# Optimization experiments

Measured on AMD Instinct MI355X. Metric: run time of the kernel, lower is better.

The kernel has to match this reference:

```python
import jax, jax.numpy as jnp
import numpy as np

B, S, E, H = 4, 2048, 1024, 16
D = E // H  # head_dim = 64
ROPE_BASE = 10000.0


def _rope(x):
    # x: [B, H, S, D] -> rotary position embedding applied over seq dim
    seq_len = x.shape[2]
    inv_freq = 1.0 / (ROPE_BASE ** (jnp.arange(0, D, 2, dtype=jnp.float32) / D))  # [D/2]
    freqs = jnp.arange(seq_len, dtype=jnp.float32)[:, None] * inv_freq[None, :]   # [S, D/2]
    emb = jnp.concatenate([freqs, freqs], axis=-1)                                 # [S, D]
    cos = jnp.cos(emb).astype(x.dtype)
    sin = jnp.sin(emb).astype(x.dtype)
    x1, x2 = jnp.split(x, 2, axis=-1)
    rotated = jnp.concatenate([-x2, x1], axis=-1)
    return x * cos + rotated * sin


def setup_inputs() -> dict:
    key = jax.random.key(0)
    ks = jax.random.split(key, 10)
    p = 0.02
    return {
        "x": jax.random.normal(ks[0], (B, S, E), dtype=jnp.float32),
        "Wq": jax.random.normal(ks[1], (E, E), dtype=jnp.float32) * p,
        "bq": jnp.zeros((E,), dtype=jnp.float32),
        "Wk": jax.random.normal(ks[2], (E, E), dtype=jnp.float32) * p,
        "bk": jnp.zeros((E,), dtype=jnp.float32),
        "Wv": jax.random.normal(ks[3], (E, E), dtype=jnp.float32) * p,
        "bv": jnp.zeros((E,), dtype=jnp.float32),
        "Wo": jax.random.normal(ks[4], (E, E), dtype=jnp.float32) * p,
        "bo": jnp.zeros((E,), dtype=jnp.float32),
        "key_padding_mask": jnp.zeros((B, S), dtype=bool),
    }


def reference(x, Wq, bq, Wk, bk, Wv, bv, Wo, bo, key_padding_mask):
    b, s, _ = x.shape
    # QKV projections -> [B, H, S, D]
    def proj(W, bias):
        return (x @ W + bias).reshape(b, s, H, D).transpose(0, 2, 1, 3)
    q = _rope(proj(Wq, bq))
    k = _rope(proj(Wk, bk))
    v = proj(Wv, bv)
    scale = D ** -0.5
    scores = jnp.einsum('bhqd,bhkd->bhqk', q, k) * scale  # [B, H, S, S]
    scores = jnp.where(key_padding_mask[:, None, None, :], jnp.finfo(scores.dtype).min, scores)
    probs = jax.nn.softmax(scores, axis=-1)
    out = jnp.einsum('bhqk,bhkd->bhqd', probs, v)         # [B, H, S, D]
    out = out.transpose(0, 2, 1, 3).reshape(b, s, E)
    return out @ Wo + bo
```

## Files before the change

### kernel.cpp

```cpp
#include <hip/hip_runtime.h>
#include <hip/hip_bf16.h>
#include <math.h>

#define Bn 4
#define Sn 2048
#define En 1024
#define Hn 16
#define Dn 64
#define Mn (Bn * Sn)

typedef __attribute__((ext_vector_type(8))) short short8;
typedef __attribute__((ext_vector_type(4))) short short4v;
typedef __attribute__((ext_vector_type(4))) float f32x4;
typedef __attribute__((ext_vector_type(16))) float f32x16;

#if __has_builtin(__builtin_amdgcn_exp2f)
#define EXP2(x) __builtin_amdgcn_exp2f(x)
#else
#define EXP2(x) exp2f(x)
#endif

#define GLOAD16(g, s) __builtin_amdgcn_global_load_lds( \
    (const __attribute__((address_space(1))) unsigned int*)(g), \
    (__attribute__((address_space(3))) unsigned int*)(s), 16, 0, 0)

__device__ inline unsigned short f2bf(float f) {
    unsigned int u = __float_as_uint(f);
    u += 0x7FFFu + ((u >> 16) & 1u);
    return (unsigned short)(u >> 16);
}
__device__ inline float bf2f(unsigned short h) {
    return __uint_as_float(((unsigned int)h) << 16);
}
__device__ inline void split2(float f, unsigned short& hi, unsigned short& lo) {
    hi = f2bf(f);
    lo = f2bf(f - bf2f(hi));
}
__device__ inline short8 ld8s(const unsigned short* p) {
    union { short4v h[2]; short8 v; } r;
    r.h[0] = *(const short4v*)p;
    r.h[1] = *(const short4v*)(p + 4);
    return r.v;
}
__device__ inline short8 g8(const unsigned short* p) {
    union { int4 i; short8 v; } r;
    r.i = *(const int4*)p;
    return r.v;
}

__device__ inline void st16(unsigned short* base, int row, int col16, int4 v) {
    const unsigned off = ((unsigned)(row * 128 + col16 * 2)) ^ ((unsigned)((row & 7) << 4));
    *(int4*)((char*)base + off) = v;
}
__device__ inline short8 ld16(const unsigned short* base, int row, int col16) {
    const unsigned off = ((unsigned)(row * 128 + col16 * 2)) ^ ((unsigned)((row & 7) << 4));
    union { int4 i; short8 v; } r;
    r.i = *(const int4*)((const char*)base + off);
    return r.v;
}

__global__ void rope_table_kernel(float* __restrict__ ct, float* __restrict__ st) {
    int i = blockIdx.x * blockDim.x + threadIdx.x;
    if (i < Sn * 32) {
        int s = i >> 5, p = i & 31;
        double inv = pow(10000.0, -(double)p / 32.0);
        double a = (double)s * inv;
        ct[i] = (float)cos(a);
        st[i] = (float)sin(a);
    }
}

__global__ __launch_bounds__(256) void convx_kernel(
    const float* __restrict__ X, unsigned short* __restrict__ Xh) {
    int i = blockIdx.x * 256 + threadIdx.x;
    float4 v = ((const float4*)X)[i];
    float f[4] = {v.x, v.y, v.z, v.w};
    short4v h;
#pragma unroll
    for (int j = 0; j < 4; ++j) h[j] = (short)f2bf(f[j]);
    ((short4v*)Xh)[i] = h;
}

__global__ __launch_bounds__(256) void tconv_kernel(
    const float* __restrict__ W, unsigned short* __restrict__ WhT,
    int rowLen, int dup) {
    __shared__ float Ws[64][65];
    const int t = threadIdx.x;
    const int kb = blockIdx.y * 64, nb = blockIdx.x * 64;
    const int lr = t >> 2, lc = (t & 3) * 16;
#pragma unroll
    for (int u = 0; u < 4; ++u) {
        float4 v = *(const float4*)&W[(size_t)(kb + lr) * En + nb + lc + 4 * u];
        Ws[lr][lc + 4 * u + 0] = v.x; Ws[lr][lc + 4 * u + 1] = v.y;
        Ws[lr][lc + 4 * u + 2] = v.z; Ws[lr][lc + 4 * u + 3] = v.w;
    }
    __syncthreads();
    const int orow = t >> 2, ock = (t & 3) * 16;
#pragma unroll
    for (int u = 0; u < 4; ++u) {
        short4v hs;
#pragma unroll
        for (int j = 0; j < 4; ++j) hs[j] = (short)f2bf(Ws[ock + 4 * u + j][orow]);
        unsigned short* dst = &WhT[(size_t)(nb + orow) * rowLen + kb + ock + 4 * u];
        *(short4v*)dst = hs;
        if (dup) *(short4v*)(dst + 1024) = hs;
    }
}

__global__ __launch_bounds__(256) void vtrans_kernel(
    const unsigned short* __restrict__ Vb, unsigned short* __restrict__ VbT) {
    __shared__ unsigned short Ts[64][68];
    const int t = threadIdx.x;
    const int bh = blockIdx.y;
    const int s0 = blockIdx.x * 64;
    const size_t ibase = (size_t)bh * Sn * Dn;
    const int lr = t >> 2, lc = (t & 3) * 16;
    int4 i0 = *(const int4*)&Vb[ibase + (size_t)(s0 + lr) * Dn + lc];
    int4 i1 = *(const int4*)&Vb[ibase + (size_t)(s0 + lr) * Dn + lc + 8];
    *(int2*)&Ts[lr][lc] = make_int2(i0.x, i0.y);
    *(int2*)&Ts[lr][lc + 4] = make_int2(i0.z, i0.w);
    *(int2*)&Ts[lr][lc + 8] = make_int2(i1.x, i1.y);
    *(int2*)&Ts[lr][lc + 12] = make_int2(i1.z, i1.w);
    __syncthreads();
    const int dr = t >> 2, sc = (t & 3) * 16;
    unsigned short o[16];
#pragma unroll
    for (int j = 0; j < 16; ++j) o[j] = Ts[sc + j][dr];
    unsigned short* op = &VbT[(size_t)bh * Dn * Sn + (size_t)dr * Sn + s0 + sc];
    *(int4*)&op[0] = *(int4*)&o[0];
    *(int4*)&op[8] = *(int4*)&o[8];
}

template <int KN, int EPI>
__global__ __launch_bounds__(256) void gemm97(
    const unsigned short* __restrict__ A, const unsigned short* __restrict__ Bt,
    const float* __restrict__ b0, const float* __restrict__ bkv,
    const float* __restrict__ bvv,
    unsigned short* __restrict__ oQ, unsigned short* __restrict__ oK,
    unsigned short* __restrict__ oV, float* __restrict__ oF,
    const float* __restrict__ ct, const float* __restrict__ st) {
    __shared__ unsigned short As[128][64];
    __shared__ unsigned short Bs[128][64];
    const int t = threadIdx.x;
    const int w = t >> 6, l = t & 63;
    const int wm = w & 1, wn = w >> 1;
    const int q = l >> 4, ln16 = l & 15;
    const int r8 = l >> 3, i8 = l & 7;
    const int m0 = blockIdx.y * 128, n0 = blockIdx.x * 128;

    f32x4 acc[4][4];
#pragma unroll
    for (int i = 0; i < 4; ++i)
#pragma unroll
        for (int j = 0; j < 4; ++j)
#pragma unroll
            for (int r = 0; r < 4; ++r) acc[i][j][r] = 0.0f;

    const unsigned short* Ag = &A[(size_t)(m0 + 32 * w + r8) * KN + 8 * i8];
    const unsigned short* Bg = &Bt[(size_t)(n0 + 32 * w + r8) * KN + 8 * i8];

    for (int k0 = 0; k0 < KN; k0 += 64) {
        __syncthreads();
#pragma unroll
        for (int j = 0; j < 4; ++j) {
            GLOAD16(Ag + (size_t)(8 * j) * KN + k0, &As[32 * w + 8 * j][0]);
            GLOAD16(Bg + (size_t)(8 * j) * KN + k0, &Bs[32 * w + 8 * j][0]);
        }
        __syncthreads();
#pragma unroll
        for (int ks = 0; ks < 2; ++ks) {
            short8 af[4], bf[4];
#pragma unroll
            for (int i = 0; i < 4; ++i)
                af[i] = ld8s(&As[64 * wm + 16 * i + ln16][32 * ks + 8 * q]);
#pragma unroll
            for (int j = 0; j < 4; ++j)
                bf[j] = ld8s(&Bs[64 * wn + 16 * j + ln16][32 * ks + 8 * q]);
#pragma unroll
            for (int i = 0; i < 4; ++i)
#pragma unroll
                for (int j = 0; j < 4; ++j)
                    acc[i][j] = __builtin_amdgcn_mfma_f32_16x16x32_bf16(
                        af[i], bf[j], acc[i][j], 0, 0, 0);
        }
    }

    if (EPI == 0) {
#pragma unroll
        for (int i = 0; i < 4; ++i)
#pragma unroll
            for (int r = 0; r < 4; ++r) {
                const int m = m0 + 64 * wm + 16 * i + 4 * q + r;
#pragma unroll
                for (int j = 0; j < 4; ++j) {
                    const int n = n0 + 64 * wn + 16 * j + ln16;
                    oF[(size_t)m * En + n] = acc[i][j][r] + b0[n];
                }
            }
    } else {
        const int mat = n0 >> 10;
        const int nIn = (n0 & 1023) + 64 * wn;
        const int hh = nIn >> 6;
        const float* bias = (mat == 0) ? b0 : (mat == 1) ? bkv : bvv;
        unsigned short* op = (mat == 0) ? oQ : (mat == 1) ? oK : oV;
#pragma unroll
        for (int i = 0; i < 4; ++i)
#pragma unroll
            for (int r = 0; r < 4; ++r) {
                const int m = m0 + 64 * wm + 16 * i + 4 * q + r;
                const int b = m >> 11, s2 = m & (Sn - 1);
                const size_t base = (((size_t)(b * Hn + hh)) * Sn + s2) * Dn;
#pragma unroll
                for (int j = 0; j < 2; ++j) {
                    const int nh = 16 * j + ln16;
                    float v0 = acc[i][j][r] + bias[nIn + nh];
                    float v1 = acc[i][j + 2][r] + bias[nIn + nh + 32];
                    if (mat <= 1) {
                        float c = ct[s2 * 32 + nh], sn = st[s2 * 32 + nh];
                        float o0 = v0 * c - v1 * sn;
                        float o1 = v1 * c + v0 * sn;
                        if (mat == 0) {
                            o0 *= 0.18033688011112042f;
                            o1 *= 0.18033688011112042f;
                        }
                        v0 = o0; v1 = o1;
                    }
                    op[base + nh] = f2bf(v0);
                    op[base + nh + 32] = f2bf(v1);
                }
            }
    }
}

__global__ __launch_bounds__(256) void attn_mfma_kernel(
    const unsigned short* __restrict__ Qb, const unsigned short* __restrict__ Kb,
    const unsigned short* __restrict__ VbT, const unsigned char* __restrict__ mask,
    unsigned short* __restrict__ Obuf) {
    __shared__ __align__(16) unsigned short Ks[2][64][64];
    __shared__ __align__(16) unsigned short Vs[2][64][64];

    const int t = threadIdx.x;
    const int w = t >> 6, l = t & 63, h2 = l >> 5, ln = l & 31;
    const int q0 = blockIdx.x * 128;
    const int h = blockIdx.y, b = blockIdx.z;
    const size_t ho = ((size_t)(b * Hn + h)) * Sn * Dn;
    const unsigned char* maskB = mask + (size_t)b * Sn;

    short8 qh[4];
    const int qrow = q0 + 32 * w + ln;
#pragma unroll
    for (int s = 0; s < 4; ++s)
        qh[s] = g8(&Qb[ho + (size_t)qrow * Dn + 16 * s + 8 * h2]);

    f32x16 accO0, accO1;
#pragma unroll
    for (int i = 0; i < 16; ++i) { accO0[i] = 0.0f; accO1[i] = 0.0f; }
    float lsum = 0.0f;

    const int kr = t >> 2, kc = (t & 3) * 16;
    const unsigned short* Kp = &Kb[ho + (size_t)kr * Dn + kc];
    const unsigned short* Vp = &VbT[ho + (size_t)kr * Sn + kc];

    int4 ck0 = *(const int4*)Kp, ck1 = *(const int4*)(Kp + 8);
    int4 cv0 = *(const int4*)Vp, cv1 = *(const int4*)(Vp + 8);
    unsigned char cm = maskB[l];

#pragma unroll 2
    for (int kt = 0; kt < Sn / 64; ++kt) {
        const int pb = kt & 1;
        unsigned short* KsP = &Ks[pb][0][0];
        unsigned short* VsP = &Vs[pb][0][0];
        st16(KsP, kr, kc, ck0); st16(KsP, kr, kc + 8, ck1);
        st16(VsP, kr, kc, cv0); st16(VsP, kr, kc + 8, cv1);
        const unsigned long long bm = __ballot(cm != 0);
        __syncthreads();
        const int kn = ((kt + 1) & (Sn / 64 - 1)) * 64;
        ck0 = *(const int4*)(Kp + (size_t)kn * Dn);
        ck1 = *(const int4*)(Kp + (size_t)kn * Dn + 8);
        cv0 = *(const int4*)(Vp + kn);
        cv1 = *(const int4*)(Vp + kn + 8);
        cm = maskB[kn + l];

#pragma unroll
        for (int c = 0; c < 2; ++c) {
            short8 kf[4];
#pragma unroll
            for (int s = 0; s < 4; ++s)
                kf[s] = ld16(KsP, 32 * c + ln, 16 * s + 8 * h2);
            f32x16 accS;
#pragma unroll
            for (int i = 0; i < 16; ++i) accS[i] = 0.0f;
            __builtin_amdgcn_s_setprio(1);
#pragma unroll
            for (int s = 0; s < 4; ++s)
                accS = __builtin_amdgcn_mfma_f32_32x32x16_bf16(kf[s], qh[s], accS, 0, 0, 0);
            __builtin_amdgcn_s_setprio(0);

            unsigned pw[8];
#pragma unroll
            for (int g = 0; g < 4; ++g)
#pragma unroll
                for (int j = 0; j < 2; ++j) {
                    const int r0 = 4 * g + 2 * j;
                    float p0 = EXP2(accS[r0]);
                    float p1 = EXP2(accS[r0 + 1]);
                    if (bm) {
                        const int key = 32 * c + 8 * g + 4 * h2 + 2 * j;
                        if ((bm >> key) & 1) p0 = 0.0f;
                        if ((bm >> (key + 1)) & 1) p1 = 0.0f;
                    }
                    const unsigned u0 = __float_as_uint(p0) & 0xFFFF0000u;
                    const unsigned u1 = __float_as_uint(p1) & 0xFFFF0000u;
                    lsum += __uint_as_float(u0);
                    lsum += __uint_as_float(u1);
                    pw[2 * g + j] = (u0 >> 16) | u1;
                }

#pragma unroll
            for (int s = 0; s < 2; ++s) {
                const unsigned x0 = pw[4 * s + 0], x1 = pw[4 * s + 1];
                const unsigned y0 = pw[4 * s + 2], y1 = pw[4 * s + 3];
                const unsigned py0 = (unsigned)__shfl_xor((int)y0, 32);
                const unsigned py1 = (unsigned)__shfl_xor((int)y1, 32);
                const unsigned px0 = (unsigned)__shfl_xor((int)x0, 32);
                const unsigned px1 = (unsigned)__shfl_xor((int)x1, 32);
                union { unsigned u[4]; short8 v; } af;
                af.u[0] = h2 ? py0 : x0;
                af.u[1] = h2 ? py1 : x1;
                af.u[2] = h2 ? y0 : px0;
                af.u[3] = h2 ? y1 : px1;
                short8 vA = ld16(VsP, ln, 32 * c + 16 * s + 8 * h2);
                short8 vB = ld16(VsP, 32 + ln, 32 * c + 16 * s + 8 * h2);
                __builtin_amdgcn_s_setprio(1);
                accO0 = __builtin_amdgcn_mfma_f32_32x32x16_bf16(af.v, vA, accO0, 0, 0, 0);
                accO1 = __builtin_amdgcn_mfma_f32_32x32x16_bf16(af.v, vB, accO1, 0, 0, 0);
                __builtin_amdgcn_s_setprio(0);
            }
        }
    }

    const float tot = lsum + __shfl_xor(lsum, 32);
    const float linv = 1.0f / fmaxf(tot, 1e-37f);
#pragma unroll
    for (int r = 0; r < 16; ++r) {
        const int row = (r & 3) + 8 * (r >> 2) + 4 * h2;
        const float lr = __shfl(linv, row);
        const int s = q0 + 32 * w + row;
        const size_t base = ((size_t)b * Sn + s) * 2048 + h * Dn;
        unsigned short a, b2;
        split2(accO0[r] * lr, a, b2);
        Obuf[base + ln] = a; Obuf[base + 1024 + ln] = b2;
        split2(accO1[r] * lr, a, b2);
        Obuf[base + 32 + ln] = a; Obuf[base + 1024 + 32 + ln] = b2;
    }
}

extern "C" void kernel_launch(void* const* d_in, const int* in_sizes, int n_in,
                              void* d_out, int out_size, void* d_ws, size_t ws_size,
                              hipStream_t stream) {
    const float* x  = (const float*)d_in[0];
    const float* Wq = (const float*)d_in[1];
    const float* bq = (const float*)d_in[2];
    const float* Wk = (const float*)d_in[3];
    const float* bk = (const float*)d_in[4];
    const float* Wv = (const float*)d_in[5];
    const float* bv = (const float*)d_in[6];
    const float* Wo = (const float*)d_in[7];
    const float* bo = (const float*)d_in[8];
    const unsigned char* mask = (const unsigned char*)d_in[9];

    const size_t NE = (size_t)Mn * En;
    const size_t WN = (size_t)En * En;
    unsigned short* ws = (unsigned short*)d_ws;
    unsigned short* Xh = ws;
    unsigned short* Qb = Xh + NE;
    unsigned short* Kb = Qb + NE;
    unsigned short* Vb = Kb + NE;
    unsigned short* VbT = Vb + NE;
    unsigned short* Obuf = VbT + NE;
    unsigned short* WqkvT = Obuf + 2 * NE;
    unsigned short* WoT2 = WqkvT + 3 * WN;
    float* ct = (float*)(WoT2 + 2 * WN);
    float* st = ct + (size_t)Sn * 32;

    rope_table_kernel<<<(Sn * 32 + 255) / 256, 256, 0, stream>>>(ct, st);
    convx_kernel<<<(int)(NE / 1024), 256, 0, stream>>>(x, Xh);
    dim3 tg(16, 16);
    tconv_kernel<<<tg, 256, 0, stream>>>(Wq, WqkvT, En, 0);
    tconv_kernel<<<tg, 256, 0, stream>>>(Wk, WqkvT + WN, En, 0);
    tconv_kernel<<<tg, 256, 0, stream>>>(Wv, WqkvT + 2 * WN, En, 0);
    tconv_kernel<<<tg, 256, 0, stream>>>(Wo, WoT2, 2048, 1);

    gemm97<En, 1><<<dim3(3 * En / 128, Mn / 128), 256, 0, stream>>>(
        Xh, WqkvT, bq, bk, bv, Qb, Kb, Vb, nullptr, ct, st);

    vtrans_kernel<<<dim3(Sn / 64, Bn * Hn), 256, 0, stream>>>(Vb, VbT);

    attn_mfma_kernel<<<dim3(Sn / 128, Hn, Bn), 256, 0, stream>>>(
        Qb, Kb, VbT, mask, Obuf);

    gemm97<2048, 0><<<dim3(En / 128, Mn / 128), 256, 0, stream>>>(
        Obuf, WoT2, bo, nullptr, nullptr, nullptr, nullptr, nullptr,
        (float*)d_out, ct, st);
}
```

Baseline: 361.0 us.

## Merge weight conversion launches, use permlane32_swap, split softmax row-sum accumulators

Replaces the four per-weight transpose/convert launches with a single launch that uses blockIdx.z to pick the weight matrix. In the attention kernel, the four cross-half shuffles plus selects are replaced by two permlane32_swap builtins when the compiler provides them. The single row-sum accumulator is split into four to shorten the dependent add chain. Launch overhead and shuffle latency are the targeted costs, and the swap path relies on builtin availability.

```diff
diff --git a/kernel.cpp b/kernel.cpp
--- a/kernel.cpp
+++ b/kernel.cpp
@@ -13,11 +13,16 @@
 typedef __attribute__((ext_vector_type(4))) short short4v;
 typedef __attribute__((ext_vector_type(4))) float f32x4;
 typedef __attribute__((ext_vector_type(16))) float f32x16;
+typedef __attribute__((ext_vector_type(2))) unsigned int uint2v;
 
 #if __has_builtin(__builtin_amdgcn_exp2f)
 #define EXP2(x) __builtin_amdgcn_exp2f(x)
 #else
 #define EXP2(x) exp2f(x)
+#endif
+
+#if __has_builtin(__builtin_amdgcn_permlane32_swap)
+#define HAVE_PLSWAP 1
 #endif
 
 #define GLOAD16(g, s) __builtin_amdgcn_global_load_lds( \
@@ -81,9 +86,16 @@
     ((short4v*)Xh)[i] = h;
 }
 
-__global__ __launch_bounds__(256) void tconv_kernel(
-    const float* __restrict__ W, unsigned short* __restrict__ WhT,
-    int rowLen, int dup) {
+__global__ __launch_bounds__(256) void tconv4_kernel(
+    const float* __restrict__ Wq, const float* __restrict__ Wk,
+    const float* __restrict__ Wv, const float* __restrict__ Wo,
+    unsigned short* __restrict__ WqkvT, unsigned short* __restrict__ WoT2) {
+    const int m = blockIdx.z;
+    const float* W = (m == 0) ? Wq : (m == 1) ? Wk : (m == 2) ? Wv : Wo;
+    unsigned short* dst = (m < 3) ? WqkvT + (size_t)m * En * En : WoT2;
+    const int rowLen = (m < 3) ? En : 2048;
+    const int dup = (m == 3);
+
     __shared__ float Ws[64][65];
     const int t = threadIdx.x;
     const int kb = blockIdx.y * 64, nb = blockIdx.x * 64;
@@ -101,9 +113,9 @@
         short4v hs;
 #pragma unroll
         for (int j = 0; j < 4; ++j) hs[j] = (short)f2bf(Ws[ock + 4 * u + j][orow]);
-        unsigned short* dst = &WhT[(size_t)(nb + orow) * rowLen + kb + ock + 4 * u];
-        *(short4v*)dst = hs;
-        if (dup) *(short4v*)(dst + 1024) = hs;
+        unsigned short* dp = &dst[(size_t)(nb + orow) * rowLen + kb + ock + 4 * u];
+        *(short4v*)dp = hs;
+        if (dup) *(short4v*)(dp + 1024) = hs;
     }
 }
 
@@ -255,7 +267,7 @@
     f32x16 accO0, accO1;
 #pragma unroll
     for (int i = 0; i < 16; ++i) { accO0[i] = 0.0f; accO1[i] = 0.0f; }
-    float lsum = 0.0f;
+    float lsum[4] = {0.0f, 0.0f, 0.0f, 0.0f};
 
     const int kr = t >> 2, kc = (t & 3) * 16;
     const unsigned short* Kp = &Kb[ho + (size_t)kr * Dn + kc];
@@ -311,24 +323,33 @@
                     }
                     const unsigned u0 = __float_as_uint(p0) & 0xFFFF0000u;
                     const unsigned u1 = __float_as_uint(p1) & 0xFFFF0000u;
-                    lsum += __uint_as_float(u0);
-                    lsum += __uint_as_float(u1);
+                    lsum[g] += __uint_as_float(u0);
+                    lsum[g] += __uint_as_float(u1);
                     pw[2 * g + j] = (u0 >> 16) | u1;
                 }
 
 #pragma unroll
             for (int s = 0; s < 2; ++s) {
+                union { unsigned u[4]; short8 v; } af;
+#ifdef HAVE_PLSWAP
+                uint2v r02 = __builtin_amdgcn_permlane32_swap(
+                    pw[4 * s + 0], pw[4 * s + 2], false, false);
+                uint2v r13 = __builtin_amdgcn_permlane32_swap(
+                    pw[4 * s + 1], pw[4 * s + 3], false, false);
+                af.u[0] = r02[0]; af.u[1] = r13[0];
+                af.u[2] = r02[1]; af.u[3] = r13[1];
+#else
                 const unsigned x0 = pw[4 * s + 0], x1 = pw[4 * s + 1];
                 const unsigned y0 = pw[4 * s + 2], y1 = pw[4 * s + 3];
                 const unsigned py0 = (unsigned)__shfl_xor((int)y0, 32);
                 const unsigned py1 = (unsigned)__shfl_xor((int)y1, 32);
                 const unsigned px0 = (unsigned)__shfl_xor((int)x0, 32);
                 const unsigned px1 = (unsigned)__shfl_xor((int)x1, 32);
-                union { unsigned u[4]; short8 v; } af;
                 af.u[0] = h2 ? py0 : x0;
                 af.u[1] = h2 ? py1 : x1;
                 af.u[2] = h2 ? y0 : px0;
                 af.u[3] = h2 ? y1 : px1;
+#endif
                 short8 vA = ld16(VsP, ln, 32 * c + 16 * s + 8 * h2);
                 short8 vB = ld16(VsP, 32 + ln, 32 * c + 16 * s + 8 * h2);
                 __builtin_amdgcn_s_setprio(1);
@@ -339,7 +360,8 @@
         }
     }
 
-    const float tot = lsum + __shfl_xor(lsum, 32);
+    const float lme = (lsum[0] + lsum[1]) + (lsum[2] + lsum[3]);
+    const float tot = lme + __shfl_xor(lme, 32);
     const float linv = 1.0f / fmaxf(tot, 1e-37f);
 #pragma unroll
     for (int r = 0; r < 16; ++r) {
@@ -385,11 +407,8 @@
 
     rope_table_kernel<<<(Sn * 32 + 255) / 256, 256, 0, stream>>>(ct, st);
     convx_kernel<<<(int)(NE / 1024), 256, 0, stream>>>(x, Xh);
-    dim3 tg(16, 16);
-    tconv_kernel<<<tg, 256, 0, stream>>>(Wq, WqkvT, En, 0);
-    tconv_kernel<<<tg, 256, 0, stream>>>(Wk, WqkvT + WN, En, 0);
-    tconv_kernel<<<tg, 256, 0, stream>>>(Wv, WqkvT + 2 * WN, En, 0);
-    tconv_kernel<<<tg, 256, 0, stream>>>(Wo, WoT2, 2048, 1);
+    tconv4_kernel<<<dim3(16, 16, 4), 256, 0, stream>>>(
+        Wq, Wk, Wv, Wo, WqkvT, WoT2);
 
     gemm97<En, 1><<<dim3(3 * En / 128, Mn / 128), 256, 0, stream>>>(
         Xh, WqkvT, bq, bk, bv, Qb, Kb, Vb, nullptr, ct, st);
```

Result: faster. 342.2 us (-5.2%).
